# Performance work log

Hardware: AMD Instinct MI355X
Metric: run time of the kernel (lower is better)

## Reference

```python
import jax, jax.numpy as jnp
import numpy as np

B, S, H, E, V, EXTRA = 256, 400, 512, 512, 50257, 100
EMB = H + E  # embedding_size


def setup_inputs() -> dict:
    key = jax.random.key(0)
    ks = jax.random.split(key, 20)
    sd = lambda *shape: 1.0 / np.sqrt(shape[-1])
    d = {
        "input_step": jax.random.normal(ks[0], (B, EMB), jnp.float32),
        "last_hidden": jax.random.normal(ks[1], (1, B, H), jnp.float32),
        "encoder_outputs": jax.random.normal(ks[2], (S, B, H), jnp.float32),
        "enc_batch_extend_vocab": jax.random.randint(ks[3], (S, B), 0, V + EXTRA, jnp.int32),
        "extra_zeros": jnp.zeros((B, EXTRA), jnp.float32),
        "attn_masks": jnp.ones((B, S), jnp.float32),
        "W_ih": jax.random.normal(ks[4], (3 * H, EMB), jnp.float32) * sd(EMB),
        "W_hh": jax.random.normal(ks[5], (3 * H, H), jnp.float32) * sd(H),
        "b_ih": jax.random.normal(ks[6], (3 * H,), jnp.float32) * 0.02,
        "b_hh": jax.random.normal(ks[7], (3 * H,), jnp.float32) * 0.02,
        "attn_W": jax.random.normal(ks[8], (H, 2 * H), jnp.float32) * sd(2 * H),
        "attn_b": jax.random.normal(ks[9], (H,), jnp.float32) * 0.02,
        "attn_v": jax.random.normal(ks[10], (H,), jnp.float32) * sd(H),
        "concat_W": jax.random.normal(ks[11], (H, 2 * H), jnp.float32) * sd(2 * H),
        "concat_b": jax.random.normal(ks[12], (H,), jnp.float32) * 0.02,
        "out_W": jax.random.normal(ks[13], (V, H), jnp.float32) * sd(H),
        "out_b": jax.random.normal(ks[14], (V,), jnp.float32) * 0.02,
        "pgen_W": jax.random.normal(ks[15], (1, 2 * H + EMB), jnp.float32) * sd(2 * H + EMB),
        "pgen_b": jax.random.normal(ks[16], (1,), jnp.float32) * 0.02,
        "sig_W": jax.random.normal(ks[17], (1, H), jnp.float32) * sd(H),
        "sig_b": jax.random.normal(ks[18], (1,), jnp.float32) * 0.02,
    }
    return d


def reference(input_step, last_hidden, encoder_outputs, enc_batch_extend_vocab,
              extra_zeros, attn_masks, W_ih, W_hh, b_ih, b_hh, attn_W, attn_b,
              attn_v, concat_W, concat_b, out_W, out_b, pgen_W, pgen_b,
              sig_W, sig_b):
    # eval-mode dropout is identity
    embedded = input_step                      # [B, EMB]
    h_prev = last_hidden[0]                    # [B, H] (nlayers = 1)

    # --- single GRU step (PyTorch gate layout: r, z, n) ---
    gi = embedded @ W_ih.T + b_ih              # [B, 3H]
    gh = h_prev @ W_hh.T + b_hh                # [B, 3H]
    i_r, i_z, i_n = jnp.split(gi, 3, axis=1)
    h_r, h_z, h_n = jnp.split(gh, 3, axis=1)
    r = jax.nn.sigmoid(i_r + h_r)
    z = jax.nn.sigmoid(i_z + h_z)
    n = jnp.tanh(i_n + r * h_n)
    rnn_output = (1.0 - z) * n + z * h_prev    # [B, H]
    hidden = rnn_output[None]                  # [1, B, H]

    # --- concat attention: v^T tanh(W [h; enc]) over source positions ---
    h_exp = jnp.broadcast_to(rnn_output[None], encoder_outputs.shape)   # [S, B, H]
    energy = jnp.tanh(
        jnp.concatenate([h_exp, encoder_outputs], axis=-1) @ attn_W.T + attn_b
    )                                          # [S, B, H]
    scores = jnp.einsum('sbh,h->bs', energy, attn_v)                    # [B, S]
    scores = jnp.where(attn_masks > 0, scores, jnp.float32(-1e18))
    attn_w = jax.nn.softmax(scores, axis=1)                             # [B, S]
    context = jnp.einsum('bs,sbh->bh', attn_w, encoder_outputs)         # [B, H]

    # --- pgen gate: sigmoid(gelu(Linear([hidden; context; emb]))) ---
    hidden_inp = h_prev                        # last_hidden flattened, [B, H]
    pgen_in = jnp.concatenate([hidden_inp, context, embedded], axis=1)
    pgen = jax.nn.sigmoid(jax.nn.gelu(pgen_in @ pgen_W.T + pgen_b,
                                      approximate=False))               # [B, 1]

    # --- vocab distribution + copy distribution, fused chain ---
    concat_out = jax.nn.gelu(
        jnp.concatenate([rnn_output, context], axis=1) @ concat_W.T + concat_b,
        approximate=False)                     # [B, H]
    logits = concat_out @ out_W.T + out_b      # [B, V]
    vocab_dist = jax.nn.softmax(logits, axis=1)
    vocab_dist = jnp.concatenate([vocab_dist, extra_zeros], axis=1)     # [B, V+EXTRA]
    vocab_dist = pgen * vocab_dist
    attn_dist = (1.0 - pgen) * attn_w          # [B, S]

    idx = enc_batch_extend_vocab.T             # [B, S]
    rows = jnp.arange(vocab_dist.shape[0])[:, None]
    final = vocab_dist.at[rows, idx].add(attn_dist)                     # scatter_add

    out = jax.nn.log_softmax(jnp.log(final + 1e-5), axis=1)

    attn_weights = attn_w.T                    # [S, B]
    sig_hid = rnn_output @ sig_W.T + sig_b     # [B, 1]
    return out, hidden, attn_weights, sig_hid
```

## Files before the change

### kernel.cpp

```cpp
#include <hip/hip_runtime.h>
#include <hip/hip_bf16.h>
#include <math.h>

#define BB 256
#define SS 400
#define HH 512
#define EMBD 1024
#define VV 50257
#define VE 50357
#define O_HID  12891392
#define O_ATT  13022464
#define O_SIG  13124864

typedef __attribute__((ext_vector_type(8))) short s8v;
typedef __attribute__((ext_vector_type(4))) float f4v;

__device__ __forceinline__ float sigmoidf(float x) { return 1.f / (1.f + expf(-x)); }
__device__ __forceinline__ float geluf(float x) { return 0.5f * x * (1.f + erff(x * 0.70710678118654752f)); }

__device__ __forceinline__ unsigned rne2_pack(float x0, float x1) {
  unsigned u0 = __float_as_uint(x0), u1 = __float_as_uint(x1);
  unsigned r0 = (u0 + 0x7FFFu + ((u0 >> 16) & 1u)) >> 16;
  unsigned r1 = (u1 + 0x7FFFu + ((u1 >> 16) & 1u)) & 0xFFFF0000u;
  return r0 | r1;
}

__device__ __forceinline__ unsigned fkey(float x) {
  unsigned u = __float_as_uint(x);
  return (u & 0x80000000u) ? ~u : (u | 0x80000000u);
}
__device__ __forceinline__ float fdecode(unsigned key) {
  unsigned u = (key & 0x80000000u) ? (key & 0x7FFFFFFFu) : ~key;
  return __uint_as_float(u);
}

template<int ACT>
__global__ __launch_bounds__(256) void gemm_nt(const float* __restrict__ A, int lda,
                                               const float* __restrict__ W, int ldw,
                                               const float* __restrict__ bias,
                                               float* __restrict__ C, int ldc,
                                               int N, int K) {
  __shared__ __align__(16) float As[16][68];
  __shared__ __align__(16) float Ws[16][68];
  const int tid = threadIdx.x;
  const int m0 = blockIdx.x * 64, n0 = blockIdx.y * 64;
  const int tx = tid & 15, ty = tid >> 4;
  const int lr = tid >> 2;
  const int lk = (tid & 3) * 4;
  float acc[4][4] = {};
  for (int k0 = 0; k0 < K; k0 += 16) {
    float4 a4, w4;
    a4 = *(const float4*)(A + (size_t)(m0 + lr) * lda + k0 + lk);
    int wrow = n0 + lr;
    if (wrow < N) w4 = *(const float4*)(W + (size_t)wrow * ldw + k0 + lk);
    else          w4 = make_float4(0.f, 0.f, 0.f, 0.f);
    __syncthreads();
    As[lk + 0][lr] = a4.x; As[lk + 1][lr] = a4.y; As[lk + 2][lr] = a4.z; As[lk + 3][lr] = a4.w;
    Ws[lk + 0][lr] = w4.x; Ws[lk + 1][lr] = w4.y; Ws[lk + 2][lr] = w4.z; Ws[lk + 3][lr] = w4.w;
    __syncthreads();
#pragma unroll
    for (int k = 0; k < 16; ++k) {
      float4 av = *(const float4*)&As[k][ty * 4];
      float4 wv = *(const float4*)&Ws[k][tx * 4];
      float am[4] = {av.x, av.y, av.z, av.w};
      float wn[4] = {wv.x, wv.y, wv.z, wv.w};
#pragma unroll
      for (int i = 0; i < 4; ++i)
#pragma unroll
        for (int j = 0; j < 4; ++j) acc[i][j] += am[i] * wn[j];
    }
  }
#pragma unroll
  for (int i = 0; i < 4; ++i) {
    int row = m0 + ty * 4 + i;
#pragma unroll
    for (int j = 0; j < 4; ++j) {
      int col = n0 + tx * 4 + j;
      if (col < N) {
        float val = acc[i][j] + bias[col];
        if (ACT == 1) val = geluf(val);
        C[(size_t)row * ldc + col] = val;
      }
    }
  }
}

__global__ __launch_bounds__(256) void gru_gemms(const float* __restrict__ input_step,
                                                 const float* __restrict__ last_hidden,
                                                 const float* __restrict__ W_ih,
                                                 const float* __restrict__ W_hh,
                                                 const float* __restrict__ b_ih,
                                                 const float* __restrict__ b_hh,
                                                 float* __restrict__ gi, float* __restrict__ gh) {
  __shared__ __align__(16) float As[16][68];
  __shared__ __align__(16) float Ws[16][68];
  const bool isGi = blockIdx.y < 24;
  const float* A = isGi ? input_step : last_hidden;
  const float* W = isGi ? W_ih : W_hh;
  const float* bias = isGi ? b_ih : b_hh;
  float* C = isGi ? gi : gh;
  const int lda = isGi ? 1024 : 512;
  const int K = isGi ? 1024 : 512;
  const int n0 = (isGi ? blockIdx.y : blockIdx.y - 24) * 64;
  const int m0 = blockIdx.x * 64;
  const int tid = threadIdx.x;
  const int tx = tid & 15, ty = tid >> 4;
  const int lr = tid >> 2;
  const int lk = (tid & 3) * 4;
  float acc[4][4] = {};
  for (int k0 = 0; k0 < K; k0 += 16) {
    float4 a4 = *(const float4*)(A + (size_t)(m0 + lr) * lda + k0 + lk);
    float4 w4 = *(const float4*)(W + (size_t)(n0 + lr) * lda + k0 + lk);
    __syncthreads();
    As[lk + 0][lr] = a4.x; As[lk + 1][lr] = a4.y; As[lk + 2][lr] = a4.z; As[lk + 3][lr] = a4.w;
    Ws[lk + 0][lr] = w4.x; Ws[lk + 1][lr] = w4.y; Ws[lk + 2][lr] = w4.z; Ws[lk + 3][lr] = w4.w;
    __syncthreads();
#pragma unroll
    for (int k = 0; k < 16; ++k) {
      float4 av = *(const float4*)&As[k][ty * 4];
      float4 wv = *(const float4*)&Ws[k][tx * 4];
      float am[4] = {av.x, av.y, av.z, av.w};
      float wn[4] = {wv.x, wv.y, wv.z, wv.w};
#pragma unroll
      for (int i = 0; i < 4; ++i)
#pragma unroll
        for (int j = 0; j < 4; ++j) acc[i][j] += am[i] * wn[j];
    }
  }
#pragma unroll
  for (int i = 0; i < 4; ++i) {
    int row = m0 + ty * 4 + i;
#pragma unroll
    for (int j = 0; j < 4; ++j) {
      int col = n0 + tx * 4 + j;
      C[(size_t)row * 1536 + col] = acc[i][j] + bias[col];
    }
  }
}

__global__ __launch_bounds__(256) void gru_combine(const float* __restrict__ gi, const float* __restrict__ gh,
                                                   const float* __restrict__ hprev,
                                                   float* __restrict__ rnn, float* __restrict__ hid_out,
                                                   float* __restrict__ cin) {
  int idx = blockIdx.x * 256 + threadIdx.x;
  int b = idx >> 9, j = idx & 511;
  const float* gib = gi + (size_t)b * 1536;
  const float* ghb = gh + (size_t)b * 1536;
  float r = sigmoidf(gib[j] + ghb[j]);
  float z = sigmoidf(gib[512 + j] + ghb[512 + j]);
  float n = tanhf(gib[1024 + j] + r * ghb[1024 + j]);
  float h = hprev[idx];
  float o = (1.f - z) * n + z * h;
  rnn[idx] = o;
  hid_out[idx] = o;
  cin[(size_t)b * 1024 + j] = o;
}

__global__ __launch_bounds__(256) void pack_rne(const float* __restrict__ src, int ld, int col0, int rows,
                                                unsigned short* __restrict__ d) {
  int idx = blockIdx.x * 256 + threadIdx.x;
  int l = idx & 63;
  int kb = (idx >> 6) & 15;
  int jb = idx >> 10;
  int j = jb * 16 + (l & 15);
  int k0 = kb * 32 + (l >> 4) * 8;
  float4 x0 = make_float4(0.f, 0.f, 0.f, 0.f), x1 = x0;
  if (j < rows) {
    const float* p = src + (size_t)j * ld + col0 + k0;
    x0 = *(const float4*)p;
    x1 = *(const float4*)(p + 4);
  }
  uint4 p = make_uint4(rne2_pack(x0.x, x0.y), rne2_pack(x0.z, x0.w),
                       rne2_pack(x1.x, x1.y), rne2_pack(x1.z, x1.w));
  *(uint4*)(d + (size_t)idx * 8) = p;
}

__global__ __launch_bounds__(256, 2) void attn_mfma(const float* __restrict__ enc,
                                                    const unsigned short* __restrict__ BP,
                                                    const float* __restrict__ hW,
                                                    const float* __restrict__ v,
                                                    float* __restrict__ scores) {
  __shared__ float sredf[64][4];

  const int tid = threadIdx.x;
  const int R0 = blockIdx.x * 64;
  const int jhalf = blockIdx.y;
  const int lane = tid & 63;
  const int w = tid >> 6;
  const int jbBase = jhalf * 16 + w * 4;
  const int g = lane >> 4;
  const int l16 = lane & 15;

  const float* a0 = enc + (size_t)(R0 + l16) * 512 + g * 8;
  const unsigned short* b0p = BP + lane * 8;

  f4v acc[4][4];
#pragma unroll
  for (int rt = 0; rt < 4; ++rt)
#pragma unroll
    for (int ct = 0; ct < 4; ++ct) acc[rt][ct] = (f4v){0.f, 0.f, 0.f, 0.f};

  s8v BH[4];
#pragma unroll
  for (int ct = 0; ct < 4; ++ct)
    BH[ct] = *(const s8v*)(b0p + ((jbBase + ct) * 16 + 0) * 512);

  for (int t = 0; t < 16; ++t) {
    const int k0 = t * 32;
    s8v af[4];
#pragma unroll
    for (int rt = 0; rt < 4; ++rt) {
      const float* ap = a0 + k0 + rt * 8192;
      float4 x0 = *(const float4*)(ap);
      float4 x1 = *(const float4*)(ap + 4);
      uint4 p = make_uint4(rne2_pack(x0.x, x0.y), rne2_pack(x0.z, x0.w),
                           rne2_pack(x1.x, x1.y), rne2_pack(x1.z, x1.w));
      af[rt] = *(s8v*)&p;
    }
#pragma unroll
    for (int rt = 0; rt < 4; ++rt)
#pragma unroll
      for (int ct = 0; ct < 4; ++ct)
        acc[rt][ct] = __builtin_amdgcn_mfma_f32_16x16x32_bf16(af[rt], BH[ct], acc[rt][ct], 0, 0, 0);
    if (t < 15) {
#pragma unroll
      for (int ct = 0; ct < 4; ++ct)
        BH[ct] = *(const s8v*)(b0p + ((jbBase + ct) * 16 + (t + 1)) * 512);
    }
  }

  float sp[4][4] = {};
#pragma unroll
  for (int ct = 0; ct < 4; ++ct) {
    int j = jhalf * 256 + w * 64 + ct * 16 + l16;
    float vj = v[j];
    const float* hWj = hW + j;
#pragma unroll
    for (int rt = 0; rt < 4; ++rt) {
#pragma unroll
      for (int q = 0; q < 4; ++q) {
        int rl = rt * 16 + g * 4 + q;
        int b = (R0 + rl) & 255;
        float e = acc[rt][ct][q] + hWj[(size_t)b * 512];
        sp[rt][q] += tanhf(e) * vj;
      }
    }
  }

#pragma unroll
  for (int rt = 0; rt < 4; ++rt)
#pragma unroll
    for (int q = 0; q < 4; ++q) {
      float s = sp[rt][q];
      s += __shfl_xor(s, 1); s += __shfl_xor(s, 2);
      s += __shfl_xor(s, 4); s += __shfl_xor(s, 8);
      if (l16 == 0) sredf[rt * 16 + g * 4 + q][w] = s;
    }
  __syncthreads();
  if (tid < 64) {
    float s = sredf[tid][0] + sredf[tid][1] + sredf[tid][2] + sredf[tid][3];
    int r = R0 + tid;
    int b = r & 255, si = r >> 8;
    atomicAdd(scores + b * 400 + si, s);
  }
}

__global__ __launch_bounds__(256, 2) void logits_mfma(const float* __restrict__ A,
                                                      const float* __restrict__ W,
                                                      const float* __restrict__ bias,
                                                      float* __restrict__ out,
                                                      unsigned* __restrict__ rowmK) {
  __shared__ __align__(16) unsigned short AL[2 * 4 * 66 * 8];

  const int tid = threadIdx.x;
  const int R0 = blockIdx.x * 64;
  const int C0 = blockIdx.y * 256;
  const int lane = tid & 63;
  const int w = tid >> 6;
  const int g = lane >> 4;
  const int l16 = lane & 15;

  const int ar = tid >> 2;
  const int akc = tid & 3;
  const float* aptr = A + (size_t)(R0 + ar) * 512 + akc * 8;

  int jc[4]; bool jok[4];
#pragma unroll
  for (int ct = 0; ct < 4; ++ct) {
    jc[ct] = C0 + w * 64 + ct * 16 + l16;
    jok[ct] = jc[ct] < VV;
  }

  f4v acc[4][4];
#pragma unroll
  for (int rt = 0; rt < 4; ++rt)
#pragma unroll
    for (int ct = 0; ct < 4; ++ct) acc[rt][ct] = (f4v){0.f, 0.f, 0.f, 0.f};

  {
    float4 pa0 = *(const float4*)(aptr);
    float4 pa1 = *(const float4*)(aptr + 4);
    uint4 p = make_uint4(rne2_pack(pa0.x, pa0.y), rne2_pack(pa0.z, pa0.w),
                         rne2_pack(pa1.x, pa1.y), rne2_pack(pa1.z, pa1.w));
    *(uint4*)&AL[(akc * 66 + ar) * 8] = p;
  }
  __syncthreads();

#pragma unroll 2
  for (int t = 0; t < 16; ++t) {
    const int k0 = t * 32;
    s8v Bf[4];
#pragma unroll
    for (int ct = 0; ct < 4; ++ct) {
      const float* wp = W + (size_t)(jok[ct] ? jc[ct] : 0) * 512 + k0 + g * 8;
      float4 b0 = *(const float4*)wp;
      float4 b1 = *(const float4*)(wp + 4);
      if (!jok[ct]) { b0 = make_float4(0.f, 0.f, 0.f, 0.f); b1 = b0; }
      uint4 pb = make_uint4(rne2_pack(b0.x, b0.y), rne2_pack(b0.z, b0.w),
                            rne2_pack(b1.x, b1.y), rne2_pack(b1.z, b1.w));
      Bf[ct] = *(s8v*)&pb;
    }
    float4 pa0, pa1;
    if (t < 15) {
      pa0 = *(const float4*)(aptr + k0 + 32);
      pa1 = *(const float4*)(aptr + k0 + 36);
    }
    const int rb = ((t & 1) * 4 + g) * 66 + l16;
#pragma unroll
    for (int rt = 0; rt < 4; ++rt) {
      s8v a = *(const s8v*)&AL[(rb + rt * 16) * 8];
#pragma unroll
      for (int ct = 0; ct < 4; ++ct)
        acc[rt][ct] = __builtin_amdgcn_mfma_f32_16x16x32_bf16(a, Bf[ct], acc[rt][ct], 0, 0, 0);
    }
    if (t < 15) {
      uint4 p = make_uint4(rne2_pack(pa0.x, pa0.y), rne2_pack(pa0.z, pa0.w),
                           rne2_pack(pa1.x, pa1.y), rne2_pack(pa1.z, pa1.w));
      *(uint4*)&AL[((((t + 1) & 1) * 4 + akc) * 66 + ar) * 8] = p;
    }
    __syncthreads();
  }

  float rmax[4][4];
#pragma unroll
  for (int rt = 0; rt < 4; ++rt)
#pragma unroll
    for (int q = 0; q < 4; ++q) rmax[rt][q] = -3e38f;
#pragma unroll
  for (int ct = 0; ct < 4; ++ct) {
    if (!jok[ct]) continue;
    float bj = bias[jc[ct]];
#pragma unroll
    for (int rt = 0; rt < 4; ++rt) {
      int row = R0 + rt * 16 + g * 4;
#pragma unroll
      for (int q = 0; q < 4; ++q) {
        float val = acc[rt][ct][q] + bj;
        out[(size_t)(row + q) * VE + jc[ct]] = val;
        rmax[rt][q] = fmaxf(rmax[rt][q], val);
      }
    }
  }
  float* redm = (float*)AL;
#pragma unroll
  for (int rt = 0; rt < 4; ++rt)
#pragma unroll
    for (int q = 0; q < 4; ++q) {
      float mx = rmax[rt][q];
      mx = fmaxf(mx, __shfl_xor(mx, 1)); mx = fmaxf(mx, __shfl_xor(mx, 2));
      mx = fmaxf(mx, __shfl_xor(mx, 4)); mx = fmaxf(mx, __shfl_xor(mx, 8));
      if (l16 == 0) redm[(rt * 16 + g * 4 + q) * 4 + w] = mx;
    }
  __syncthreads();
  if (tid < 64) {
    float mx = fmaxf(fmaxf(redm[tid * 4 + 0], redm[tid * 4 + 1]),
                     fmaxf(redm[tid * 4 + 2], redm[tid * 4 + 3]));
    if (mx > -2e38f) atomicMax(rowmK + R0 + tid, fkey(mx));
  }
}

__global__ __launch_bounds__(256) void softmax_k(const float* __restrict__ scores,
                                                 const float* __restrict__ masks,
                                                 float* __restrict__ attnw, float* __restrict__ attnT) {
  int b = blockIdx.x, tid = threadIdx.x;
  __shared__ float red[4];
  float m = -3e38f;
  for (int s = tid; s < 400; s += 256) {
    float sc = (masks[b * 400 + s] > 0.f) ? scores[b * 400 + s] : -1e18f;
    m = fmaxf(m, sc);
  }
#pragma unroll
  for (int o = 32; o; o >>= 1) m = fmaxf(m, __shfl_xor(m, o));
  if ((tid & 63) == 0) red[tid >> 6] = m;
  __syncthreads();
  m = fmaxf(fmaxf(red[0], red[1]), fmaxf(red[2], red[3]));
  __syncthreads();
  float z = 0.f;
  for (int s = tid; s < 400; s += 256) {
    float sc = (masks[b * 400 + s] > 0.f) ? scores[b * 400 + s] : -1e18f;
    z += expf(sc - m);
  }
#pragma unroll
  for (int o = 32; o; o >>= 1) z += __shfl_xor(z, o);
  if ((tid & 63) == 0) red[tid >> 6] = z;
  __syncthreads();
  z = red[0] + red[1] + red[2] + red[3];
  float inv = 1.f / z;
  for (int s = tid; s < 400; s += 256) {
    float sc = (masks[b * 400 + s] > 0.f) ? scores[b * 400 + s] : -1e18f;
    float w = expf(sc - m) * inv;
    attnw[b * 400 + s] = w;
    attnT[s * 256 + b] = w;
  }
}

__global__ __launch_bounds__(1024) void context_pgen_k(const float* __restrict__ enc,
                                                       const float* __restrict__ attnw,
                                                       const float* __restrict__ hprev,
                                                       const float* __restrict__ emb,
                                                       const float* __restrict__ pW,
                                                       const float* __restrict__ pb,
                                                       float* __restrict__ ctx, float* __restrict__ cin,
                                                       float* __restrict__ pgen) {
  int b = blockIdx.x, tid = threadIdx.x;
  __shared__ float w[400];
  __shared__ float part[4][512];
  __shared__ float red[16];
  for (int s = tid; s < 400; s += 1024) w[s] = attnw[b * 400 + s];
  __syncthreads();
  const int h = (tid & 255) * 2;
  const int sq = tid >> 8;
  const float* p = enc + (size_t)b * 512 + h;
  float cx = 0.f, cy = 0.f;
  const int s0 = sq * 100;
#pragma unroll 4
  for (int s = s0; s < s0 + 100; ++s) {
    float2 e = *(const float2*)(p + (size_t)s * 131072);
    cx += w[s] * e.x; cy += w[s] * e.y;
  }
  part[sq][h] = cx; part[sq][h + 1] = cy;
  __syncthreads();
  float vsum = 0.f;
  if (tid < 512) {
    vsum = part[0][tid] + part[1][tid] + part[2][tid] + part[3][tid];
    ctx[(size_t)b * 512 + tid] = vsum;
    cin[(size_t)b * 1024 + 512 + tid] = vsum;
  }
  __syncthreads();
  if (tid < 512) part[0][tid] = vsum;
  __syncthreads();
  float acc = 0.f;
#pragma unroll
  for (int kk = 0; kk < 2; ++kk) {
    int k = tid + kk * 1024;
    float x = (k < 512) ? hprev[(size_t)b * 512 + k]
            : (k < 1024) ? part[0][k - 512]
            : emb[(size_t)b * 1024 + k - 1024];
    acc += x * pW[k];
  }
#pragma unroll
  for (int o = 32; o; o >>= 1) acc += __shfl_xor(acc, o);
  if ((tid & 63) == 0) red[tid >> 6] = acc;
  __syncthreads();
  if (tid == 0) {
    float d = pb[0];
#pragma unroll
    for (int i = 0; i < 16; ++i) d += red[i];
    pgen[b] = sigmoidf(geluf(d));
  }
}

__global__ void sig_k(const float* __restrict__ rnn, const float* __restrict__ sW,
                      const float* __restrict__ sb, float* __restrict__ outp) {
  int b = blockIdx.x, tid = threadIdx.x;
  float acc = 0.f;
  for (int k = tid; k < 512; k += 64) acc += rnn[(size_t)b * 512 + k] * sW[k];
#pragma unroll
  for (int o = 32; o; o >>= 1) acc += __shfl_xor(acc, o);
  if (tid == 0) outp[b] = acc + sb[0];
}

__global__ __launch_bounds__(1024) void finale_k(float* __restrict__ out,
                                                 const float* __restrict__ pgen,
                                                 const unsigned* __restrict__ rowmK,
                                                 const int* __restrict__ ebev,
                                                 const float* __restrict__ attnw) {
  const int b = blockIdx.x, tid = threadIdx.x;
  float* row = out + (size_t)b * VE;
  __shared__ float red[16];
  __shared__ float shZ;
  const float m = fdecode(rowmK[b]);
  const float pg = pgen[b];
  float z = 0.f;
  for (int j = tid * 4; j < 50356; j += 4096) {
    float4 x = *(const float4*)(row + j);
    float4 e;
    e.x = (j + 0 < VV) ? expf(x.x - m) : 0.f;
    e.y = (j + 1 < VV) ? expf(x.y - m) : 0.f;
    e.z = (j + 2 < VV) ? expf(x.z - m) : 0.f;
    e.w = (j + 3 < VV) ? expf(x.w - m) : 0.f;
    z += e.x + e.y + e.z + e.w;
    *(float4*)(row + j) = e;
  }
  if (tid == 0) row[50356] = 0.f;
#pragma unroll
  for (int o = 32; o; o >>= 1) z += __shfl_xor(z, o);
  if ((tid & 63) == 0) red[tid >> 6] = z;
  __syncthreads();
  if (tid == 0) {
    float t = 0.f;
#pragma unroll
    for (int i = 0; i < 16; ++i) t += red[i];
    shZ = t;
  }
  __syncthreads();
  const float coef = pg / shZ;
  if (tid < 400) {
    int idx = ebev[tid * 256 + b];
    float wv = (1.f - pg) * attnw[b * 400 + tid] / coef;
    atomicAdd(row + idx, wv);
  }
  __syncthreads();
  const float logT = logf(1.0f + (float)VE * 1e-5f);
  volatile const float* vrow = row;
  for (int j = tid; j < VE; j += 1024) {
    float e = vrow[j];
    row[j] = logf(coef * e + 1e-5f) - logT;
  }
}

extern "C" void kernel_launch(void* const* d_in, const int* in_sizes, int n_in,
                              void* d_out, int out_size, void* d_ws, size_t ws_size,
                              hipStream_t stream) {
  const float* input_step = (const float*)d_in[0];
  const float* last_hidden = (const float*)d_in[1];
  const float* enc = (const float*)d_in[2];
  const int*   ebev = (const int*)d_in[3];
  const float* masks = (const float*)d_in[5];
  const float* W_ih = (const float*)d_in[6];
  const float* W_hh = (const float*)d_in[7];
  const float* b_ih = (const float*)d_in[8];
  const float* b_hh = (const float*)d_in[9];
  const float* attn_W = (const float*)d_in[10];
  const float* attn_b = (const float*)d_in[11];
  const float* attn_v = (const float*)d_in[12];
  const float* concat_W = (const float*)d_in[13];
  const float* concat_b = (const float*)d_in[14];
  const float* out_W = (const float*)d_in[15];
  const float* out_b = (const float*)d_in[16];
  const float* pgen_W = (const float*)d_in[17];
  const float* pgen_b = (const float*)d_in[18];
  const float* sig_W = (const float*)d_in[19];
  const float* sig_b = (const float*)d_in[20];

  float* out = (float*)d_out;
  float* ws = (float*)d_ws;
  float* gi     = ws;
  float* gh     = gi + 393216;
  float* rnn    = gh + 393216;
  float* hW     = rnn + 131072;
  float* scores = hW + 131072;
  float* attnw  = scores + 102400;
  float* ctx    = attnw + 102400;
  float* cin    = ctx + 131072;
  float* cout_  = cin + 262144;
  float* pgen   = cout_ + 131072;
  float* rowm   = pgen + 256;
  float* coef   = rowm + 256;
  float* logT   = coef + 256;
  unsigned short* Bhi = (unsigned short*)(logT + 256);
  unsigned short* Blo = Bhi + 262144;

  pack_rne<<<128, 256, 0, stream>>>(attn_W, 1024, 512, 512, Bhi);
  hipMemsetAsync(scores, 0, 102400 * sizeof(float), stream);
  hipMemsetAsync(rowm, 0, 256 * sizeof(float), stream);
  gru_gemms<<<dim3(4, 48), 256, 0, stream>>>(input_step, last_hidden, W_ih, W_hh, b_ih, b_hh, gi, gh);
  gru_combine<<<512, 256, 0, stream>>>(gi, gh, last_hidden, rnn, out + O_HID, cin);
  gemm_nt<0><<<dim3(4, 8), 256, 0, stream>>>(rnn, 512, attn_W, 1024, attn_b, hW, 512, 512, 512);
  attn_mfma<<<dim3(1600, 2), 256, 0, stream>>>(enc, Bhi, hW, attn_v, scores);
  softmax_k<<<256, 256, 0, stream>>>(scores, masks, attnw, out + O_ATT);
  context_pgen_k<<<256, 1024, 0, stream>>>(enc, attnw, last_hidden, input_step,
                                           pgen_W, pgen_b, ctx, cin, pgen);
  sig_k<<<256, 64, 0, stream>>>(rnn, sig_W, sig_b, out + O_SIG);
  gemm_nt<1><<<dim3(4, 8), 256, 0, stream>>>(cin, 1024, concat_W, 1024, concat_b, cout_, 512, 512, 1024);
  logits_mfma<<<dim3(4, 197), 256, 0, stream>>>(cout_, out_W, out_b, out, (unsigned*)rowm);
  finale_k<<<256, 1024, 0, stream>>>(out, pgen, (const unsigned*)rowm, ebev, attnw);
}
```

Measured before the change: 634.2 us.

## Stage attention encoder tile in LDS with double buffering and smaller tiles

The attention-score MFMA kernel now loads each encoder A tile cooperatively once per block, converts it to bf16, and stores it in a double-buffered shared-memory buffer. Before, each wave loaded and converted its own copy from global memory. The per-block tile shrinks from 64 rows × 256 columns to 32 rows × 128 columns, so the grid grows to 3200×4 and launch bounds go up to 8 blocks per CU for more occupancy. In exchange, the encoder tensor is re-read by four column blocks instead of two, and there is a barrier every k-step and more atomic adds into scores.

```diff
diff --git a/kernel.cpp b/kernel.cpp
--- a/kernel.cpp
+++ b/kernel.cpp
@@ -175,68 +175,78 @@
   *(uint4*)(d + (size_t)idx * 8) = p;
 }
 
-__global__ __launch_bounds__(256, 2) void attn_mfma(const float* __restrict__ enc,
+__global__ __launch_bounds__(256, 8) void attn_mfma(const float* __restrict__ enc,
                                                     const unsigned short* __restrict__ BP,
                                                     const float* __restrict__ hW,
                                                     const float* __restrict__ v,
                                                     float* __restrict__ scores) {
-  __shared__ float sredf[64][4];
+  __shared__ __align__(16) unsigned short AL[2 * 4 * 34 * 8];
+  __shared__ float sredf[32][4];
 
   const int tid = threadIdx.x;
-  const int R0 = blockIdx.x * 64;
-  const int jhalf = blockIdx.y;
+  const int R0 = blockIdx.x * 32;
+  const int jquad = blockIdx.y;
   const int lane = tid & 63;
   const int w = tid >> 6;
-  const int jbBase = jhalf * 16 + w * 4;
+  const int jbBase = jquad * 8 + w * 2;
   const int g = lane >> 4;
   const int l16 = lane & 15;
 
-  const float* a0 = enc + (size_t)(R0 + l16) * 512 + g * 8;
+  const int ar = tid >> 3;
+  const int kc4 = tid & 7;
+  const int akc = kc4 >> 1;
+  const int ahalf = kc4 & 1;
+  const float* aptr = enc + (size_t)(R0 + ar) * 512 + kc4 * 4;
+
   const unsigned short* b0p = BP + lane * 8;
 
-  f4v acc[4][4];
-#pragma unroll
-  for (int rt = 0; rt < 4; ++rt)
-#pragma unroll
-    for (int ct = 0; ct < 4; ++ct) acc[rt][ct] = (f4v){0.f, 0.f, 0.f, 0.f};
-
-  s8v BH[4];
-#pragma unroll
-  for (int ct = 0; ct < 4; ++ct)
+  f4v acc[2][2];
+#pragma unroll
+  for (int rt = 0; rt < 2; ++rt)
+#pragma unroll
+    for (int ct = 0; ct < 2; ++ct) acc[rt][ct] = (f4v){0.f, 0.f, 0.f, 0.f};
+
+  {
+    float4 x = *(const float4*)(aptr);
+    uint2 p = make_uint2(rne2_pack(x.x, x.y), rne2_pack(x.z, x.w));
+    *(uint2*)&AL[((akc * 34 + ar) * 8) + ahalf * 4] = p;
+  }
+  s8v BH[2];
+#pragma unroll
+  for (int ct = 0; ct < 2; ++ct)
     BH[ct] = *(const s8v*)(b0p + ((jbBase + ct) * 16 + 0) * 512);
+  __syncthreads();
 
   for (int t = 0; t < 16; ++t) {
     const int k0 = t * 32;
-    s8v af[4];
-#pragma unroll
-    for (int rt = 0; rt < 4; ++rt) {
-      const float* ap = a0 + k0 + rt * 8192;
-      float4 x0 = *(const float4*)(ap);
-      float4 x1 = *(const float4*)(ap + 4);
-      uint4 p = make_uint4(rne2_pack(x0.x, x0.y), rne2_pack(x0.z, x0.w),
-                           rne2_pack(x1.x, x1.y), rne2_pack(x1.z, x1.w));
-      af[rt] = *(s8v*)&p;
-    }
-#pragma unroll
-    for (int rt = 0; rt < 4; ++rt)
-#pragma unroll
-      for (int ct = 0; ct < 4; ++ct)
-        acc[rt][ct] = __builtin_amdgcn_mfma_f32_16x16x32_bf16(af[rt], BH[ct], acc[rt][ct], 0, 0, 0);
+    float4 pa;
+    if (t < 15) pa = *(const float4*)(aptr + k0 + 32);
+    const int rb = ((t & 1) * 4 + g) * 34 + l16;
+#pragma unroll
+    for (int rt = 0; rt < 2; ++rt) {
+      s8v a = *(const s8v*)&AL[(rb + rt * 16) * 8];
+#pragma unroll
+      for (int ct = 0; ct < 2; ++ct)
+        acc[rt][ct] = __builtin_amdgcn_mfma_f32_16x16x32_bf16(a, BH[ct], acc[rt][ct], 0, 0, 0);
+    }
     if (t < 15) {
 #pragma unroll
-      for (int ct = 0; ct < 4; ++ct)
+      for (int ct = 0; ct < 2; ++ct)
         BH[ct] = *(const s8v*)(b0p + ((jbBase + ct) * 16 + (t + 1)) * 512);
-    }
-  }
-
-  float sp[4][4] = {};
-#pragma unroll
-  for (int ct = 0; ct < 4; ++ct) {
-    int j = jhalf * 256 + w * 64 + ct * 16 + l16;
+      uint2 p = make_uint2(rne2_pack(pa.x, pa.y), rne2_pack(pa.z, pa.w));
+      *(uint2*)&AL[((((t + 1) & 1) * 4 + akc) * 34 + ar) * 8 + ahalf * 4] = p;
+    }
+    __syncthreads();
+  }
+
+  float sp[2][4] = {};
+#pragma unroll
+  for (int ct = 0; ct < 2; ++ct) {
+    int j = jquad * 128 + w * 32 + ct * 16 + l16;
     float vj = v[j];
     const float* hWj = hW + j;
 #pragma unroll
-    for (int rt = 0; rt < 4; ++rt) {
+    for (int rt = 0; rt < 2; ++rt) {
 #pragma unroll
       for (int q = 0; q < 4; ++q) {
         int rl = rt * 16 + g * 4 + q;
@@ -248,7 +258,7 @@
   }
 
 #pragma unroll
-  for (int rt = 0; rt < 4; ++rt)
+  for (int rt = 0; rt < 2; ++rt)
 #pragma unroll
     for (int q = 0; q < 4; ++q) {
       float s = sp[rt][q];
@@ -257,7 +267,7 @@
       if (l16 == 0) sredf[rt * 16 + g * 4 + q][w] = s;
     }
   __syncthreads();
-  if (tid < 64) {
+  if (tid < 32) {
     float s = sredf[tid][0] + sredf[tid][1] + sredf[tid][2] + sredf[tid][3];
     int r = R0 + tid;
     int b = r & 255, si = r >> 8;
@@ -577,7 +587,7 @@
   gru_gemms<<<dim3(4, 48), 256, 0, stream>>>(input_step, last_hidden, W_ih, W_hh, b_ih, b_hh, gi, gh);
   gru_combine<<<512, 256, 0, stream>>>(gi, gh, last_hidden, rnn, out + O_HID, cin);
   gemm_nt<0><<<dim3(4, 8), 256, 0, stream>>>(rnn, 512, attn_W, 1024, attn_b, hW, 512, 512, 512);
-  attn_mfma<<<dim3(1600, 2), 256, 0, stream>>>(enc, Bhi, hW, attn_v, scores);
+  attn_mfma<<<dim3(3200, 4), 256, 0, stream>>>(enc, Bhi, hW, attn_v, scores);
   softmax_k<<<256, 256, 0, stream>>>(scores, masks, attnw, out + O_ATT);
   context_pgen_k<<<256, 1024, 0, stream>>>(enc, attnw, last_hidden, input_step,
                                            pgen_W, pgen_b, ctx, cin, pgen);
```

Measured after the change: 509.3 us. 19.7% less time.
